# Kernel tuning notes

Hardware: AMD Instinct MI355X
Metric: run time of the kernel (lower is better)

Reference implementation:

```python
import jax, jax.numpy as jnp
import numpy as np

D_MODEL = 768
N_HEADS = 12
HEAD_DIM = D_MODEL // N_HEADS
NEG = -10000.0


def setup_inputs() -> dict:
    key = jax.random.key(0)
    ks = jax.random.split(key, 8)
    B, S, D = 2, 2048, D_MODEL
    inp = {
        "q": jax.random.normal(ks[0], (B, S, D), dtype=jnp.float32),
        "k": jax.random.normal(ks[1], (B, S, D), dtype=jnp.float32),
        "v": jax.random.normal(ks[2], (B, S, D), dtype=jnp.float32),
        "attn_mask": jax.random.randint(ks[3], (B, S), 0, 2, dtype=jnp.int32),
        # weights stored [in, out]; apply as x @ W (equivalent to torch Linear)
        "Wq": jax.random.normal(ks[4], (D, D), dtype=jnp.float32) / np.sqrt(D),
        "Wk": jax.random.normal(ks[5], (D, D), dtype=jnp.float32) / np.sqrt(D),
        "Wv": jax.random.normal(ks[6], (D, D), dtype=jnp.float32) / np.sqrt(D),
        "Wo": jax.random.normal(ks[7], (D, D), dtype=jnp.float32) / np.sqrt(D),
        "mask_future": 1,
    }
    return inp


def reference(q, k, v, attn_mask, Wq, Wk, Wv, Wo, mask_future):
    B, S, D = q.shape
    H, hd = N_HEADS, HEAD_DIM
    # project and split heads -> [B, H, S, hd]
    qh = (q @ Wq).reshape(B, S, H, hd).transpose(0, 2, 1, 3)
    kh = (k @ Wk).reshape(B, S, H, hd).transpose(0, 2, 1, 3)
    vh = (v @ Wv).reshape(B, S, H, hd).transpose(0, 2, 1, 3)

    scale = 1.0 / np.sqrt(hd).astype(np.float32)
    # full [B, H, L, S] score matrix (naive SDPA, as in the original)
    scores = jnp.einsum("bhld,bhsd->bhls", qh, kh) * scale
    if mask_future:
        causal = jnp.triu(jnp.full((S, S), NEG, dtype=scores.dtype), k=1)
        scores = scores + causal
    # padding mask: [B, S] -> broadcast over heads and query positions
    pad = attn_mask[:, None, None, :] == 0
    scores = jnp.where(pad, NEG, scores)
    attn = jax.nn.softmax(scores, axis=-1)  # dropout p=0.0 -> identity
    out = jnp.einsum("bhls,bhsd->bhld", attn, vh)  # [B, H, L, hd]
    out = out.transpose(0, 2, 1, 3).reshape(B, S, D)
    return out @ Wo
```

## Files before the change

kernel.cpp:

```cpp
#include <hip/hip_runtime.h>


#define NEGV (-10000.0f)

typedef __attribute__((ext_vector_type(8))) short v8s;
typedef __attribute__((ext_vector_type(4))) float v4f;
typedef __attribute__((ext_vector_type(8))) unsigned short v8u;

__device__ __forceinline__ unsigned short f2bf(float f) {
  unsigned int u = __float_as_uint(f);
  u += 0x7FFFu + ((u >> 16) & 1u);
  return (unsigned short)(u >> 16);
}

__global__ __launch_bounds__(256) void transpose_w(
    const float* __restrict__ w0, const float* __restrict__ w1,
    const float* __restrict__ w2, const float* __restrict__ w3,
    unsigned short* __restrict__ t0, unsigned short* __restrict__ t1,
    unsigned short* __restrict__ t2, unsigned short* __restrict__ t3) {
  const float* w; unsigned short* t;
  switch (blockIdx.z) {
    case 0: w = w0; t = t0; break;
    case 1: w = w1; t = t1; break;
    case 2: w = w2; t = t2; break;
    default: w = w3; t = t3; break;
  }
  __shared__ unsigned short tile[32][33];
  const int tx = threadIdx.x & 31, ty = threadIdx.x >> 5;
  const int x0 = blockIdx.x * 32, y0 = blockIdx.y * 32;
#pragma unroll
  for (int j = 0; j < 4; j++)
    tile[ty + j * 8][tx] = f2bf(w[(size_t)(y0 + ty + j * 8) * 768 + x0 + tx]);
  __syncthreads();
#pragma unroll
  for (int j = 0; j < 4; j++)
    t[(size_t)(x0 + ty + j * 8) * 768 + y0 + tx] = tile[tx][ty + j * 8];
}

template <bool ABF16HEAD, bool CF32ROW>
__device__ __forceinline__ void gemm_core(const void* __restrict__ A,
                                          const unsigned short* __restrict__ Wt,
                                          void* __restrict__ C) {
  const int tid = threadIdx.x;
  const int wave = tid >> 6, lane = tid & 63;
  const int quad = lane >> 4, l16 = lane & 15;
  const int wm = wave >> 1, wn = wave & 1;
  const int bm = blockIdx.x * 128, bn = blockIdx.y * 128;

  __shared__ __align__(16) unsigned short As[128 * 32];
  __shared__ __align__(16) unsigned short Bs[128 * 32];

  v4f acc[4][4];
#pragma unroll
  for (int i = 0; i < 4; i++)
#pragma unroll
    for (int j = 0; j < 4; j++) acc[i][j] = (v4f){0.f, 0.f, 0.f, 0.f};

  for (int kt = 0; kt < 24; kt++) {
    __syncthreads();
#pragma unroll
    for (int p = 0; p < 2; p++) {
      int idx = p * 256 + tid;
      int r = idx >> 2, c0 = (idx & 3) << 3;
      int rg = bm + r, c = kt * 32 + c0;
      if (ABF16HEAD) {
        size_t aoff = ((size_t)((rg >> 11) * 12 + (c >> 6)) * 2048 +
                       (rg & 2047)) * 64 + (c & 63);
        *(uint4*)&As[r * 32 + c0] =
            *(const uint4*)((const unsigned short*)A + aoff);
      } else {
        const float* Af = (const float*)A;
        size_t aoff = (size_t)rg * 768 + c;
        float4 x0 = *(const float4*)(Af + aoff);
        float4 x1 = *(const float4*)(Af + aoff + 4);
        v8u tmp;
        tmp[0] = f2bf(x0.x); tmp[1] = f2bf(x0.y);
        tmp[2] = f2bf(x0.z); tmp[3] = f2bf(x0.w);
        tmp[4] = f2bf(x1.x); tmp[5] = f2bf(x1.y);
        tmp[6] = f2bf(x1.z); tmp[7] = f2bf(x1.w);
        *(uint4*)&As[r * 32 + c0] = *(uint4*)&tmp;
      }
      *(uint4*)&Bs[r * 32 + c0] =
          *(const uint4*)&Wt[(size_t)(bn + r) * 768 + c];
    }
    __syncthreads();

    v8s aF[4], bF[4];
#pragma unroll
    for (int mt = 0; mt < 4; mt++)
      aF[mt] = *(const v8s*)&As[(wm * 64 + mt * 16 + l16) * 32 + quad * 8];
#pragma unroll
    for (int nt = 0; nt < 4; nt++)
      bF[nt] = *(const v8s*)&Bs[(wn * 64 + nt * 16 + l16) * 32 + quad * 8];
#pragma unroll
    for (int mt = 0; mt < 4; mt++)
#pragma unroll
      for (int nt = 0; nt < 4; nt++)
        acc[mt][nt] = __builtin_amdgcn_mfma_f32_16x16x32_bf16(
            aF[mt], bF[nt], acc[mt][nt], 0, 0, 0);
  }

#pragma unroll
  for (int mt = 0; mt < 4; mt++) {
#pragma unroll
    for (int i = 0; i < 4; i++) {
      int row = bm + wm * 64 + mt * 16 + quad * 4 + i;
#pragma unroll
      for (int nt = 0; nt < 4; nt++) {
        int col = bn + wn * 64 + nt * 16 + l16;
        if (CF32ROW) {
          ((float*)C)[(size_t)row * 768 + col] = acc[mt][nt][i];
        } else {
          size_t off = ((size_t)((row >> 11) * 12 + (col >> 6)) * 2048 +
                        (row & 2047)) * 64 + (col & 63);
          ((unsigned short*)C)[off] = f2bf(acc[mt][nt][i]);
        }
      }
    }
  }
}

__global__ __launch_bounds__(256) void gemm_qkv(
    const float* __restrict__ xq, const float* __restrict__ xk,
    const float* __restrict__ xv, const unsigned short* __restrict__ wqt,
    const unsigned short* __restrict__ wkt, const unsigned short* __restrict__ wvt,
    unsigned short* __restrict__ qh, unsigned short* __restrict__ kh,
    unsigned short* __restrict__ vh) {
  const float* A; const unsigned short* Wt; unsigned short* C;
  switch (blockIdx.z) {
    case 0: A = xq; Wt = wqt; C = qh; break;
    case 1: A = xk; Wt = wkt; C = kh; break;
    default: A = xv; Wt = wvt; C = vh; break;
  }
  gemm_core<false, false>((const void*)A, Wt, (void*)C);
}

__global__ __launch_bounds__(256) void gemm_o(
    const unsigned short* __restrict__ oat, const unsigned short* __restrict__ wot,
    float* __restrict__ out) {
  gemm_core<true, true>((const void*)oat, wot, (void*)out);
}

__global__ __launch_bounds__(256) void attn_kernel(
    const unsigned short* __restrict__ qh, const unsigned short* __restrict__ kh,
    const unsigned short* __restrict__ vh, const int* __restrict__ attn_mask,
    const int* __restrict__ mask_future, unsigned short* __restrict__ o) {
  const int S = 2048, HD = 64, NH = 12;
  const int qt = blockIdx.x;
  const int bh = blockIdx.y;
  const int b = bh / NH, h = bh % NH;
  const int tid = threadIdx.x;
  const int wave = tid >> 6, lane = tid & 63;
  const int quad = lane >> 4, l16 = lane & 15;

  __shared__ __align__(16) unsigned short Ks[64 * 72];
  __shared__ __align__(16) unsigned short Vt[64 * 72];
  __shared__ __align__(16) unsigned short Ps[4][16 * 72];
  __shared__ int Ms[64];
  __shared__ int s_flag;

  const size_t head_off = (size_t)(b * NH + h) * S * HD;
  const unsigned short* Kb = kh + head_off;
  const unsigned short* Vb = vh + head_off;

  const int mf = mask_future[0];
  if (tid == 0) s_flag = 0;

  const int qrowA = qt * 64 + wave * 16 + l16;
  v8s aQ[2];
  {
    const unsigned short* qp = qh + head_off + (size_t)qrowA * HD + quad * 8;
    aQ[0] = *(const v8s*)(qp);
    aQ[1] = *(const v8s*)(qp + 32);
  }
  const int qbase = qt * 64 + wave * 16 + quad * 4;

  float m_i[4], l_i[4];
  v4f accO[4];
#pragma unroll
  for (int i = 0; i < 4; i++) { m_i[i] = -1e30f; l_i[i] = 0.f; }
#pragma unroll
  for (int dt = 0; dt < 4; dt++) accO[dt] = (v4f){0.f, 0.f, 0.f, 0.f};

  const int kt_causal = mf ? qt : (S / 64 - 1);

  for (int phase = 0; phase < 2; phase++) {
    int kt_lo, kt_hi;
    if (phase == 0) { kt_lo = 0; kt_hi = kt_causal; }
    else {
      bool need = (m_i[0] < -5000.f) || (m_i[1] < -5000.f) ||
                  (m_i[2] < -5000.f) || (m_i[3] < -5000.f);
      if (need) s_flag = 1;
      __syncthreads();
      if (!s_flag) break;
      kt_lo = kt_causal + 1; kt_hi = S / 64 - 1;
    }
    for (int kt = kt_lo; kt <= kt_hi; kt++) {
      __syncthreads();
      {
        const uint4* srck = (const uint4*)(Kb + (size_t)kt * 64 * HD);
        const uint4* srcv = (const uint4*)(Vb + (size_t)kt * 64 * HD);
#pragma unroll
        for (int p = 0; p < 2; p++) {
          int idx = p * 256 + tid;
          int r = idx >> 3;
          int c0 = (idx & 7) << 3;
          *(uint4*)&Ks[r * 72 + c0] = srck[idx];
          v8u vv;
          *(uint4*)&vv = srcv[idx];
          int shift = (idx & 7) << 3;
#pragma unroll
          for (int i = 0; i < 8; i++) {
            int d = c0 + i;
            int scol = (r + shift) & 63;
            Vt[d * 72 + scol] = vv[i];
          }
        }
        if (tid < 64) Ms[tid] = attn_mask[b * S + kt * 64 + tid];
      }
      __syncthreads();

      v4f sc[4];
#pragma unroll
      for (int nt = 0; nt < 4; nt++) {
        const unsigned short* kp = &Ks[(nt * 16 + l16) * 72 + quad * 8];
        v8s b0 = *(const v8s*)kp;
        v8s b1 = *(const v8s*)(kp + 32);
        v4f z = (v4f){0.f, 0.f, 0.f, 0.f};
        z = __builtin_amdgcn_mfma_f32_16x16x32_bf16(aQ[0], b0, z, 0, 0, 0);
        z = __builtin_amdgcn_mfma_f32_16x16x32_bf16(aQ[1], b1, z, 0, 0, 0);
        sc[nt] = z;
      }

#pragma unroll
      for (int nt = 0; nt < 4; nt++) {
        int key = kt * 64 + nt * 16 + l16;
        bool pad = (Ms[nt * 16 + l16] == 0);
#pragma unroll
        for (int i = 0; i < 4; i++) {
          float v = sc[nt][i] * 0.125f;
          v += (mf && (key > qbase + i)) ? NEGV : 0.f;
          v = pad ? NEGV : v;
          sc[nt][i] = v;
        }
      }

#pragma unroll
      for (int i = 0; i < 4; i++) {
        float mx = fmaxf(fmaxf(sc[0][i], sc[1][i]), fmaxf(sc[2][i], sc[3][i]));
        mx = fmaxf(mx, __shfl_xor(mx, 1));
        mx = fmaxf(mx, __shfl_xor(mx, 2));
        mx = fmaxf(mx, __shfl_xor(mx, 4));
        mx = fmaxf(mx, __shfl_xor(mx, 8));
        float mnew = fmaxf(m_i[i], mx);
        float alpha = __expf(m_i[i] - mnew);
        m_i[i] = mnew;
        float rs = 0.f;
#pragma unroll
        for (int nt = 0; nt < 4; nt++) {
          float p = __expf(sc[nt][i] - mnew);
          sc[nt][i] = p;
          rs += p;
        }
        rs += __shfl_xor(rs, 1);
        rs += __shfl_xor(rs, 2);
        rs += __shfl_xor(rs, 4);
        rs += __shfl_xor(rs, 8);
        l_i[i] = l_i[i] * alpha + rs;
#pragma unroll
        for (int dt = 0; dt < 4; dt++) accO[dt][i] *= alpha;
      }

#pragma unroll
      for (int nt = 0; nt < 4; nt++)
#pragma unroll
        for (int i = 0; i < 4; i++)
          Ps[wave][(quad * 4 + i) * 72 + nt * 16 + l16] = f2bf(sc[nt][i]);

#pragma unroll
      for (int ks = 0; ks < 2; ks++) {
        v8s aP = *(const v8s*)&Ps[wave][l16 * 72 + ks * 32 + quad * 8];
#pragma unroll
        for (int dt = 0; dt < 4; dt++) {
          int d = dt * 16 + l16;
          int scol = ((ks * 32 + quad * 8) + ((d >> 3) << 3)) & 63;
          v8s bV = *(const v8s*)&Vt[d * 72 + scol];
          accO[dt] =
              __builtin_amdgcn_mfma_f32_16x16x32_bf16(aP, bV, accO[dt], 0, 0, 0);
        }
      }
    }
    if (phase == 0) __syncthreads();
  }

#pragma unroll
  for (int i = 0; i < 4; i++) {
    float inv = 1.f / l_i[i];
    int qr = qbase + i;
    size_t base = head_off + (size_t)qr * HD;
#pragma unroll
    for (int dt = 0; dt < 4; dt++)
      o[base + dt * 16 + l16] = f2bf(accO[dt][i] * inv);
  }
}

extern "C" void kernel_launch(void* const* d_in, const int* in_sizes, int n_in,
                              void* d_out, int out_size, void* d_ws, size_t ws_size,
                              hipStream_t stream) {
  const float* q  = (const float*)d_in[0];
  const float* k  = (const float*)d_in[1];
  const float* v  = (const float*)d_in[2];
  const int* amask = (const int*)d_in[3];
  const float* Wq = (const float*)d_in[4];
  const float* Wk = (const float*)d_in[5];
  const float* Wv = (const float*)d_in[6];
  const float* Wo = (const float*)d_in[7];
  const int* mf  = (const int*)d_in[8];
  float* out = (float*)d_out;

  unsigned short* ws = (unsigned short*)d_ws;
  unsigned short* qh = ws;
  unsigned short* kh = qh + 3145728;
  unsigned short* vh = kh + 3145728;
  unsigned short* wqt = vh + 3145728;
  unsigned short* wkt = wqt + 589824;
  unsigned short* wvt = wkt + 589824;
  unsigned short* wot = wvt + 589824;

  transpose_w<<<dim3(24, 24, 4), 256, 0, stream>>>(Wq, Wk, Wv, Wo,
                                                   wqt, wkt, wvt, wot);
  gemm_qkv<<<dim3(32, 6, 3), 256, 0, stream>>>(q, k, v, wqt, wkt, wvt,
                                               qh, kh, vh);
  attn_kernel<<<dim3(32, 24), 256, 0, stream>>>(qh, kh, vh, amask, mf, qh);
  gemm_o<<<dim3(32, 6), 256, 0, stream>>>(qh, wot, out);
}
```

Before: 246.7 us.

## Prefetch global tiles into registers, halve GEMM M-tile, reverse attention block order

Both the GEMM and attention kernels now load the next K-tile (weights/activations, or K/V/mask) into registers right after the barrier, so global latency overlaps the MFMA work on the current tile. The GEMM M-tile is halved to 64 rows and the grid doubled, which gives more blocks for 256 CUs. Attention processes the heaviest causal query tiles first by reversing blockIdx.x, which should balance the tail. The costs are extra register pressure and a lower compute-to-load ratio per GEMM block.

Result: no change. 248.2 us (+0.6%).

```diff
diff --git a/kernel.cpp b/kernel.cpp
--- a/kernel.cpp
+++ b/kernel.cpp
@@ -45,55 +45,66 @@
   const int wave = tid >> 6, lane = tid & 63;
   const int quad = lane >> 4, l16 = lane & 15;
   const int wm = wave >> 1, wn = wave & 1;
-  const int bm = blockIdx.x * 128, bn = blockIdx.y * 128;
-
-  __shared__ __align__(16) unsigned short As[128 * 32];
+  const int bm = blockIdx.x * 64, bn = blockIdx.y * 128;
+
+  __shared__ __align__(16) unsigned short As[64 * 32];
   __shared__ __align__(16) unsigned short Bs[128 * 32];
 
-  v4f acc[4][4];
-#pragma unroll
-  for (int i = 0; i < 4; i++)
+  v4f acc[2][4];
+#pragma unroll
+  for (int i = 0; i < 2; i++)
 #pragma unroll
     for (int j = 0; j < 4; j++) acc[i][j] = (v4f){0.f, 0.f, 0.f, 0.f};
 
+  const int ar = tid >> 2, ac0 = (tid & 3) << 3;
+  const int brr = tid >> 2, bc0 = (tid & 3) << 3;
+
+  float4 pa0, pa1; uint4 pabf; uint4 pb0, pb1;
+
+  auto prefetch = [&](int kt) {
+    int c = kt * 32 + ac0;
+    if (ABF16HEAD) {
+      int rg = bm + ar;
+      size_t aoff = ((size_t)((rg >> 11) * 12 + (c >> 6)) * 2048 +
+                     (rg & 2047)) * 64 + (c & 63);
+      pabf = *(const uint4*)((const unsigned short*)A + aoff);
+    } else {
+      const float* Af = (const float*)A;
+      size_t aoff = (size_t)(bm + ar) * 768 + c;
+      pa0 = *(const float4*)(Af + aoff);
+      pa1 = *(const float4*)(Af + aoff + 4);
+    }
+    pb0 = *(const uint4*)&Wt[(size_t)(bn + brr) * 768 + kt * 32 + bc0];
+    pb1 = *(const uint4*)&Wt[(size_t)(bn + 64 + brr) * 768 + kt * 32 + bc0];
+  };
+
+  prefetch(0);
   for (int kt = 0; kt < 24; kt++) {
     __syncthreads();
-#pragma unroll
-    for (int p = 0; p < 2; p++) {
-      int idx = p * 256 + tid;
-      int r = idx >> 2, c0 = (idx & 3) << 3;
-      int rg = bm + r, c = kt * 32 + c0;
-      if (ABF16HEAD) {
-        size_t aoff = ((size_t)((rg >> 11) * 12 + (c >> 6)) * 2048 +
-                       (rg & 2047)) * 64 + (c & 63);
-        *(uint4*)&As[r * 32 + c0] =
-            *(const uint4*)((const unsigned short*)A + aoff);
-      } else {
-        const float* Af = (const float*)A;
-        size_t aoff = (size_t)rg * 768 + c;
-        float4 x0 = *(const float4*)(Af + aoff);
-        float4 x1 = *(const float4*)(Af + aoff + 4);
-        v8u tmp;
-        tmp[0] = f2bf(x0.x); tmp[1] = f2bf(x0.y);
-        tmp[2] = f2bf(x0.z); tmp[3] = f2bf(x0.w);
-        tmp[4] = f2bf(x1.x); tmp[5] = f2bf(x1.y);
-        tmp[6] = f2bf(x1.z); tmp[7] = f2bf(x1.w);
-        *(uint4*)&As[r * 32 + c0] = *(uint4*)&tmp;
-      }
-      *(uint4*)&Bs[r * 32 + c0] =
-          *(const uint4*)&Wt[(size_t)(bn + r) * 768 + c];
-    }
+    if (ABF16HEAD) {
+      *(uint4*)&As[ar * 32 + ac0] = pabf;
+    } else {
+      v8u tmp;
+      tmp[0] = f2bf(pa0.x); tmp[1] = f2bf(pa0.y);
+      tmp[2] = f2bf(pa0.z); tmp[3] = f2bf(pa0.w);
+      tmp[4] = f2bf(pa1.x); tmp[5] = f2bf(pa1.y);
+      tmp[6] = f2bf(pa1.z); tmp[7] = f2bf(pa1.w);
+      *(uint4*)&As[ar * 32 + ac0] = *(uint4*)&tmp;
+    }
+    *(uint4*)&Bs[brr * 32 + bc0] = pb0;
+    *(uint4*)&Bs[(64 + brr) * 32 + bc0] = pb1;
     __syncthreads();
-
-    v8s aF[4], bF[4];
-#pragma unroll
-    for (int mt = 0; mt < 4; mt++)
-      aF[mt] = *(const v8s*)&As[(wm * 64 + mt * 16 + l16) * 32 + quad * 8];
+    if (kt < 23) prefetch(kt + 1);
+
+    v8s aF[2], bF[4];
+#pragma unroll
+    for (int mt = 0; mt < 2; mt++)
+      aF[mt] = *(const v8s*)&As[(wm * 32 + mt * 16 + l16) * 32 + quad * 8];
 #pragma unroll
     for (int nt = 0; nt < 4; nt++)
       bF[nt] = *(const v8s*)&Bs[(wn * 64 + nt * 16 + l16) * 32 + quad * 8];
 #pragma unroll
-    for (int mt = 0; mt < 4; mt++)
+    for (int mt = 0; mt < 2; mt++)
 #pragma unroll
       for (int nt = 0; nt < 4; nt++)
         acc[mt][nt] = __builtin_amdgcn_mfma_f32_16x16x32_bf16(
@@ -101,10 +112,10 @@
   }
 
 #pragma unroll
-  for (int mt = 0; mt < 4; mt++) {
+  for (int mt = 0; mt < 2; mt++) {
 #pragma unroll
     for (int i = 0; i < 4; i++) {
-      int row = bm + wm * 64 + mt * 16 + quad * 4 + i;
+      int row = bm + wm * 32 + mt * 16 + quad * 4 + i;
 #pragma unroll
       for (int nt = 0; nt < 4; nt++) {
         int col = bn + wn * 64 + nt * 16 + l16;
@@ -146,7 +157,7 @@
     const unsigned short* __restrict__ vh, const int* __restrict__ attn_mask,
     const int* __restrict__ mask_future, unsigned short* __restrict__ o) {
   const int S = 2048, HD = 64, NH = 12;
-  const int qt = blockIdx.x;
+  const int qt = 31 - blockIdx.x;
   const int bh = blockIdx.y;
   const int b = bh / NH, h = bh % NH;
   const int tid = threadIdx.x;
@@ -183,6 +194,18 @@
   for (int dt = 0; dt < 4; dt++) accO[dt] = (v4f){0.f, 0.f, 0.f, 0.f};
 
   const int kt_causal = mf ? qt : (S / 64 - 1);
+
+  const int r0 = tid >> 3, c00 = (tid & 7) << 3;
+  const int r1 = (256 + tid) >> 3, c01 = ((256 + tid) & 7) << 3;
+  uint4 pK0, pK1, pV0, pV1;
+  int pM;
+  auto prefetch = [&](int kt) {
+    const uint4* srck = (const uint4*)(Kb + (size_t)kt * 64 * HD);
+    const uint4* srcv = (const uint4*)(Vb + (size_t)kt * 64 * HD);
+    pK0 = srck[tid];       pK1 = srck[256 + tid];
+    pV0 = srcv[tid];       pV1 = srcv[256 + tid];
+    if (tid < 64) pM = attn_mask[b * S + kt * 64 + tid];
+  };
 
   for (int phase = 0; phase < 2; phase++) {
     int kt_lo, kt_hi;
@@ -194,31 +217,27 @@
       __syncthreads();
       if (!s_flag) break;
       kt_lo = kt_causal + 1; kt_hi = S / 64 - 1;
-    }
+      if (kt_lo > kt_hi) break;
+    }
+    prefetch(kt_lo);
     for (int kt = kt_lo; kt <= kt_hi; kt++) {
       __syncthreads();
       {
-        const uint4* srck = (const uint4*)(Kb + (size_t)kt * 64 * HD);
-        const uint4* srcv = (const uint4*)(Vb + (size_t)kt * 64 * HD);
-#pragma unroll
-        for (int p = 0; p < 2; p++) {
-          int idx = p * 256 + tid;
-          int r = idx >> 3;
-          int c0 = (idx & 7) << 3;
-          *(uint4*)&Ks[r * 72 + c0] = srck[idx];
-          v8u vv;
-          *(uint4*)&vv = srcv[idx];
-          int shift = (idx & 7) << 3;
-#pragma unroll
-          for (int i = 0; i < 8; i++) {
-            int d = c0 + i;
-            int scol = (r + shift) & 63;
-            Vt[d * 72 + scol] = vv[i];
-          }
-        }
-        if (tid < 64) Ms[tid] = attn_mask[b * S + kt * 64 + tid];
+        *(uint4*)&Ks[r0 * 72 + c00] = pK0;
+        *(uint4*)&Ks[r1 * 72 + c01] = pK1;
+        v8u vv0 = *(v8u*)&pV0;
+        v8u vv1 = *(v8u*)&pV1;
+        int sh0 = (tid & 7) << 3, sh1 = ((256 + tid) & 7) << 3;
+#pragma unroll
+        for (int i = 0; i < 8; i++) {
+          int d0 = c00 + i, d1 = c01 + i;
+          Vt[d0 * 72 + ((r0 + sh0) & 63)] = vv0[i];
+          Vt[d1 * 72 + ((r1 + sh1) & 63)] = vv1[i];
+        }
+        if (tid < 64) Ms[tid] = pM;
       }
       __syncthreads();
+      if (kt < kt_hi) prefetch(kt + 1);
 
       v4f sc[4];
 #pragma unroll
@@ -329,8 +348,8 @@
 
   transpose_w<<<dim3(24, 24, 4), 256, 0, stream>>>(Wq, Wk, Wv, Wo,
                                                    wqt, wkt, wvt, wot);
-  gemm_qkv<<<dim3(32, 6, 3), 256, 0, stream>>>(q, k, v, wqt, wkt, wvt,
+  gemm_qkv<<<dim3(64, 6, 3), 256, 0, stream>>>(q, k, v, wqt, wkt, wvt,
                                                qh, kh, vh);
   attn_kernel<<<dim3(32, 24), 256, 0, stream>>>(qh, kh, vh, amask, mf, qh);
-  gemm_o<<<dim3(32, 6), 256, 0, stream>>>(qh, wot, out);
-}
+  gemm_o<<<dim3(64, 6), 256, 0, stream>>>(qh, wot, out);
+}
```
